# Optimization experiments

Hardware: AMD Instinct MI355X
Metric: run time of the kernel (lower is better)

## Reference

```python
import jax, jax.numpy as jnp
import numpy as np

N = 50000      # num nodes
E = 800000     # num edges (avg degree 16)
IN, H, OUT = 128, 128, 16
R = 8          # num relations


def rgcn_conv(x, edge_index, edge_type, W, root, bias, num_relations):
    """PyG RGCNConv with aggr='mean': out = x@root + bias + sum_r mean_{j in N_r(i)} x_j @ W_r.
    Mean is linear, so aggregate raw x_j per relation first, then one matmul per relation."""
    src, dst = edge_index[0], edge_index[1]  # messages flow src -> dst
    x_src = x[src]                            # [E, F] gather
    out = x @ root + bias                     # root/self term
    for r in range(num_relations):            # small fixed loop over relations
        m = (edge_type == r).astype(x.dtype)  # [E]
        s = jax.ops.segment_sum(x_src * m[:, None], dst, num_segments=x.shape[0])  # [N, F]
        c = jax.ops.segment_sum(m, dst, num_segments=x.shape[0])                   # [N]
        out = out + (s / jnp.maximum(c, 1.0)[:, None]) @ W[r]
    return out


def setup_inputs() -> dict:
    key = jax.random.key(0)
    ks = jax.random.split(key, 12)
    glorot = lambda k, shape: jax.random.normal(k, shape, jnp.float32) * (2.0 / (shape[-2] + shape[-1])) ** 0.5
    return {
        "x": jax.random.normal(ks[0], (N, IN), jnp.float32),
        "edge_index": jax.random.randint(ks[1], (2, E), 0, N, jnp.int64) if jax.config.read('jax_enable_x64') else jax.random.randint(ks[1], (2, E), 0, N).astype(jnp.int32),
        "edge_type": jax.random.randint(ks[2], (E,), 0, R).astype(jnp.int32),
        "w0": glorot(ks[3], (R, IN, H)),
        "root0": glorot(ks[4], (IN, H)),
        "b0": jnp.zeros((H,), jnp.float32),
        "w1": glorot(ks[5], (R, H, H)),
        "root1": glorot(ks[6], (H, H)),
        "b1": jnp.zeros((H,), jnp.float32),
        "w2": glorot(ks[7], (R, H, OUT)),
        "root2": glorot(ks[8], (H, OUT)),
        "b2": jnp.zeros((OUT,), jnp.float32),
    }


def reference(x, edge_index, edge_type, w0, root0, b0, w1, root1, b1, w2, root2, b2):
    # layer 0: in -> hidden, relu (dropout is identity in eval mode)
    h = jax.nn.relu(rgcn_conv(x, edge_index, edge_type, w0, root0, b0, R))
    # layer 1: hidden -> hidden, relu
    h = jax.nn.relu(rgcn_conv(h, edge_index, edge_type, w1, root1, b1, R))
    # layer 2: hidden -> out (no activation)
    return rgcn_conv(h, edge_index, edge_type, w2, root2, b2, R)
```

## Files before the change

kernel.cpp:

```cpp
#include <hip/hip_runtime.h>

#define N_NODES 50000
#define N_EDGES 800000
#define NREL 8
#define NB8 (N_NODES * NREL)
#define SCAN_T 12500
#define KSTEPS 36
#define A_STRIDE 1160
#define NTILES (N_NODES / 16)

typedef __attribute__((ext_vector_type(8))) short short8;
typedef __attribute__((ext_vector_type(4))) float f32x4;
typedef __attribute__((ext_vector_type(2))) float f32x2;

__device__ __forceinline__ unsigned short f2bf(float v) {
    union { float f; unsigned int u; } c; c.f = v;
    return (unsigned short)((c.u + 0x7FFFu + ((c.u >> 16) & 1u)) >> 16);
}
__device__ __forceinline__ float bfhi2f(unsigned int u) {
    union { unsigned int u; float f; } c; c.u = u & 0xFFFF0000u; return c.f;
}
__device__ __forceinline__ float bflo2f(unsigned int u) {
    union { unsigned int u; float f; } c; c.u = u << 16; return c.f;
}

#define PREP_Z   (NB8 / 4)
#define PREP_X   (N_NODES * 32)
#define PREP_P   (8 * KSTEPS * 64)
#define PREP_P2  (1 * KSTEPS * 64)
#define PREP_TOTAL (PREP_Z + PREP_X + 2 * PREP_P + PREP_P2)

__device__ __forceinline__ void pack_one(int idx, const float* __restrict__ root,
                                         const float* __restrict__ W,
                                         unsigned short* __restrict__ Wpack, int FOUT) {
    int lane = idx & 63;
    int ks = (idx >> 6) % KSTEPS;
    int ct = idx / (KSTEPS * 64);
    int kbase = ks * 32 + (lane >> 4) * 8;
    int col = ct * 16 + (lane & 15);
    union { unsigned short us[8]; uint4 v; } u;
#pragma unroll
    for (int j = 0; j < 8; j++) {
        int k = kbase + j;
        float val = (k < 128) ? root[(size_t)k * FOUT + col]
                              : W[(size_t)(k - 128) * FOUT + col];
        u.us[j] = f2bf(val);
    }
    ((uint4*)Wpack)[idx] = u.v;
}

__global__ void prep_kernel(const float* __restrict__ X, unsigned int* __restrict__ Xb2,
                            const float* __restrict__ r0, const float* __restrict__ w0,
                            unsigned short* __restrict__ Wp0,
                            const float* __restrict__ r1, const float* __restrict__ w1,
                            unsigned short* __restrict__ Wp1,
                            const float* __restrict__ r2, const float* __restrict__ w2,
                            unsigned short* __restrict__ Wp2,
                            int* __restrict__ cnt) {
    int t = blockIdx.x * blockDim.x + threadIdx.x;
    if (t < PREP_Z) { ((int4*)cnt)[t] = make_int4(0, 0, 0, 0); return; }
    t -= PREP_Z;
    if (t < PREP_X) {
        float4 v = ((const float4*)X)[t];
        unsigned int p0 = (unsigned int)f2bf(v.x) | ((unsigned int)f2bf(v.y) << 16);
        unsigned int p1 = (unsigned int)f2bf(v.z) | ((unsigned int)f2bf(v.w) << 16);
        ((uint2*)Xb2)[t] = make_uint2(p0, p1);
        return;
    }
    t -= PREP_X;
    if (t < PREP_P) { pack_one(t, r0, w0, Wp0, 128); return; }
    t -= PREP_P;
    if (t < PREP_P) { pack_one(t, r1, w1, Wp1, 128); return; }
    t -= PREP_P;
    if (t < PREP_P2) pack_one(t, r2, w2, Wp2, 16);
}

__global__ void rank_kernel(const int* __restrict__ ei, const int* __restrict__ et,
                            int* __restrict__ cnt, int* __restrict__ rank, int E) {
    int e = blockIdx.x * blockDim.x + threadIdx.x;
    if (e >= E) return;
    int d = ei[E + e];
    int t = et[e];
    rank[e] = atomicAdd(&cnt[d * NREL + t], 1);
}

__global__ void scanA_kernel(const int* __restrict__ cnt, int* __restrict__ tsum) {
    int g = blockIdx.x * blockDim.x + threadIdx.x;
    if (g >= SCAN_T) return;
    const int4* p = (const int4*)(cnt + (size_t)g * 32);
    int s = 0;
#pragma unroll
    for (int j = 0; j < 8; j++) {
        int4 v = p[j];
        s += v.x + v.y + v.z + v.w;
    }
    tsum[g] = s;
}

__global__ void scanB_kernel(const int* __restrict__ tsum, int* __restrict__ toff) {
    __shared__ int part[1024];
    int t = threadIdx.x;
    const int C = 13;
    int n0 = t * C, n1 = n0 + C; if (n1 > SCAN_T) n1 = SCAN_T;
    int s = 0;
    for (int n = n0; n < n1; n++) s += tsum[n];
    part[t] = s;
    __syncthreads();
    for (int off = 1; off < 1024; off <<= 1) {
        int v = (t >= off) ? part[t - off] : 0;
        __syncthreads();
        part[t] += v;
        __syncthreads();
    }
    int run = (t > 0) ? part[t - 1] : 0;
    for (int n = n0; n < n1; n++) { toff[n] = run; run += tsum[n]; }
}

__global__ void scanC_kernel(const int* __restrict__ cnt, const int* __restrict__ toff,
                             int* __restrict__ rs8) {
    int g = blockIdx.x * blockDim.x + threadIdx.x;
    if (g >= SCAN_T) return;
    int run = toff[g];
    int base = g * 32;
#pragma unroll 4
    for (int j = 0; j < 32; j++) {
        rs8[base + j] = run;
        run += cnt[base + j];
    }
    if (g == 0) rs8[NB8] = N_EDGES;
}

__global__ void place_kernel(const int* __restrict__ ei, const int* __restrict__ et,
                             const int* __restrict__ rank, const int* __restrict__ rs8,
                             unsigned short* __restrict__ csr_src, int E) {
    int e = blockIdx.x * blockDim.x + threadIdx.x;
    if (e >= E) return;
    int s = ei[e];
    int d = ei[E + e];
    int t = et[e];
    csr_src[rs8[d * NREL + t] + rank[e]] = (unsigned short)s;
}

template <int FOUT, bool RELU>
__global__ __launch_bounds__(512, 8) void layer_kernel(
    const unsigned int* __restrict__ Xb2,
    const int* __restrict__ rs8,
    const unsigned short* __restrict__ csr_src,
    const unsigned short* __restrict__ Wpack,
    const float* __restrict__ bias,
    void* __restrict__ Yout)
{
    __shared__ __align__(16) unsigned short Abuf[16][A_STRIDE];

    int tid = threadIdx.x;
    int wave = tid >> 6, lane = tid & 63;
    int l15 = lane & 15;
    int node0 = blockIdx.x * 16;

    {
        int gn0 = node0 + wave * 2;
        unsigned int* row0 = (unsigned int*)&Abuf[wave * 2][0];
        unsigned int* row1 = (unsigned int*)&Abuf[wave * 2 + 1][0];

        int bl = lane <= 16 ? lane : 16;
        int bv = rs8[gn0 * 8 + bl];
        unsigned int self0 = Xb2[(size_t)gn0 * 64 + lane];
        unsigned int self1 = Xb2[(size_t)(gn0 + 1) * 64 + lane];

        int e     = __builtin_amdgcn_readlane(bv, 0);
        int e_end = __builtin_amdgcn_readlane(bv, 16);

        row0[lane] = self0;
        row1[lane] = self1;

        int r = 0;
        int segs = e;
        int be = __builtin_amdgcn_readlane(bv, 1);
        f32x2 av = (f32x2){0.f, 0.f};

#define FLUSH_R()                                                              \
        do {                                                                   \
            int c_ = be - segs;                                                \
            float iv_ = 1.0f / (float)(c_ > 0 ? c_ : 1);                       \
            unsigned int pk_ = (unsigned int)f2bf(av.x * iv_)                  \
                             | ((unsigned int)f2bf(av.y * iv_) << 16);         \
            unsigned int* rw_ = (r < 8) ? row0 : row1;                         \
            rw_[(1 + (r & 7)) * 64 + lane] = pk_;                              \
            av = (f32x2){0.f, 0.f}; segs = be; r++;                            \
            be = __builtin_amdgcn_readlane(bv, r + 1 <= 16 ? r + 1 : 16);      \
        } while (0)

        if (e < e_end) {
            int e1m = e_end - 1;
            int ma = e + l15; if (ma > e1m) ma = e1m;
            unsigned int mv = csr_src[ma];
            while (e < e_end) {
                int bn = e_end - e; if (bn > 16) bn = 16;
                int sc[16];
#pragma unroll
                for (int k = 0; k < 16; k++) sc[k] = __builtin_amdgcn_readlane((int)mv, k);
                unsigned int xp[16];
#pragma unroll
                for (int k = 0; k < 16; k++) xp[k] = Xb2[(size_t)sc[k] * 64 + lane];
                int en = e + bn;
                if (en < e_end) {
                    int mb = en + l15; if (mb > e1m) mb = e1m;
                    mv = csr_src[mb];
                }
#pragma unroll
                for (int k = 0; k < 16; k++) {
                    if (k < bn) {
                        int ec = e + k;
                        while (ec >= be) FLUSH_R();
                        av += (f32x2){bflo2f(xp[k]), bfhi2f(xp[k])};
                    }
                }
                e = en;
            }
        }
        while (r < 16) FLUSH_R();
#undef FLUSH_R
    }
    __syncthreads();

    int quad = lane >> 4, l16 = lane & 15;
    if constexpr (FOUT == 128) {
        int ct = wave;
        f32x4 acc = (f32x4){0.f, 0.f, 0.f, 0.f};
        for (int ks = 0; ks < KSTEPS; ks++) {
            short8 b = *(const short8*)(Wpack + (((size_t)ct * KSTEPS + ks) * 64 + lane) * 8);
            short8 a = *(const short8*)&Abuf[l16][ks * 32 + quad * 8];
            acc = __builtin_amdgcn_mfma_f32_16x16x32_bf16(a, b, acc, 0, 0, 0);
        }
        unsigned short* Yb = (unsigned short*)Yout;
        int h = ct * 16 + l16;
        float bvs = bias[h];
#pragma unroll
        for (int r4 = 0; r4 < 4; r4++) {
            int node = node0 + quad * 4 + r4;
            float v = acc[r4] + bvs;
            if (RELU) v = v > 0.f ? v : 0.f;
            Yb[(size_t)node * 128 + h] = f2bf(v);
        }
    } else {
        int ks0 = wave * 4 + (wave < 4 ? wave : 4);
        int ksn = (wave < 4) ? 5 : 4;
        f32x4 acc = (f32x4){0.f, 0.f, 0.f, 0.f};
        for (int ks = ks0; ks < ks0 + ksn; ks++) {
            short8 b = *(const short8*)(Wpack + ((size_t)ks * 64 + lane) * 8);
            short8 a = *(const short8*)&Abuf[l16][ks * 32 + quad * 8];
            acc = __builtin_amdgcn_mfma_f32_16x16x32_bf16(a, b, acc, 0, 0, 0);
        }
        __syncthreads();
        float* red = (float*)&Abuf[0][0];
#pragma unroll
        for (int r4 = 0; r4 < 4; r4++) red[(wave * 64 + lane) * 4 + r4] = acc[r4];
        __syncthreads();
        if (tid < 256) {
            int reg = tid >> 6, l = tid & 63;
            float s = 0.f;
#pragma unroll
            for (int w = 0; w < 8; w++) s += red[(w * 64 + l) * 4 + reg];
            int node = node0 + ((l >> 4) << 2) + reg;
            int h = l & 15;
            float v = s + bias[h];
            if (RELU) v = v > 0.f ? v : 0.f;
            ((float*)Yout)[(size_t)node * 16 + h] = v;
        }
    }
}

extern "C" void kernel_launch(void* const* d_in, const int* in_sizes, int n_in,
                              void* d_out, int out_size, void* d_ws, size_t ws_size,
                              hipStream_t stream) {
    const float* x  = (const float*)d_in[0];
    const int*   ei = (const int*)d_in[1];
    const int*   et = (const int*)d_in[2];
    const float* w0 = (const float*)d_in[3];
    const float* r0 = (const float*)d_in[4];
    const float* b0 = (const float*)d_in[5];
    const float* w1 = (const float*)d_in[6];
    const float* r1 = (const float*)d_in[7];
    const float* b1 = (const float*)d_in[8];
    const float* w2 = (const float*)d_in[9];
    const float* r2 = (const float*)d_in[10];
    const float* b2 = (const float*)d_in[11];

    char* wsp = (char*)d_ws;
    size_t off = 0;
    auto alloc = [&](size_t bytes) -> void* {
        void* p = wsp + off;
        off += (bytes + 255) & ~(size_t)255;
        return p;
    };

    int* cnt    = (int*)alloc((size_t)NB8 * 4);
    int* rs8    = (int*)alloc(((size_t)NB8 + 1) * 4);
    int* rank   = (int*)alloc((size_t)N_EDGES * 4);
    int* tsum   = (int*)alloc((size_t)SCAN_T * 4);
    int* toff   = (int*)alloc((size_t)SCAN_T * 4);
    unsigned short* csr_src = (unsigned short*)alloc((size_t)N_EDGES * 2);
    unsigned short* Wp0 = (unsigned short*)alloc((size_t)8 * KSTEPS * 64 * 8 * 2);
    unsigned short* Wp1 = (unsigned short*)alloc((size_t)8 * KSTEPS * 64 * 8 * 2);
    unsigned short* Wp2 = (unsigned short*)alloc((size_t)1 * KSTEPS * 64 * 8 * 2);
    unsigned int* Xb = (unsigned int*)alloc((size_t)N_NODES * 64 * 4);
    unsigned int* H0 = (unsigned int*)alloc((size_t)N_NODES * 64 * 4);
    unsigned int* H1 = (unsigned int*)alloc((size_t)N_NODES * 64 * 4);

    prep_kernel<<<dim3((PREP_TOTAL + 255) / 256), dim3(256), 0, stream>>>(
        x, Xb, r0, w0, Wp0, r1, w1, Wp1, r2, w2, Wp2, cnt);
    rank_kernel<<<dim3((N_EDGES + 255) / 256), dim3(256), 0, stream>>>(ei, et, cnt, rank, N_EDGES);
    scanA_kernel<<<dim3((SCAN_T + 255) / 256), dim3(256), 0, stream>>>(cnt, tsum);
    scanB_kernel<<<dim3(1), dim3(1024), 0, stream>>>(tsum, toff);
    scanC_kernel<<<dim3((SCAN_T + 255) / 256), dim3(256), 0, stream>>>(cnt, toff, rs8);
    place_kernel<<<dim3((N_EDGES + 255) / 256), dim3(256), 0, stream>>>(ei, et, rank, rs8,
                                                                        csr_src, N_EDGES);

    layer_kernel<128, true ><<<dim3(NTILES), dim3(512), 0, stream>>>(
        Xb, rs8, csr_src, Wp0, b0, (void*)H0);
    layer_kernel<128, true ><<<dim3(NTILES), dim3(512), 0, stream>>>(
        H0, rs8, csr_src, Wp1, b1, (void*)H1);
    layer_kernel<16, false><<<dim3(NTILES), dim3(512), 0, stream>>>(
        H1, rs8, csr_src, Wp2, b2, d_out);
}
```

Baseline: 322.4 us.

## Warp-specialize layer kernel with double-buffered producer/consumer tiles and fuse scan kernels

The layer kernel now processes several 16-node tiles per block. Four producer waves gather and mean-aggregate neighbour features into one of two shared buffers while four consumer waves run the MFMA GEMM on the other buffer. The aim is to overlap gather latency with matrix math and to drop the cross-wave reduction in the FOUT=16 layer. Separately, the three scan kernels become one kernel that uses global atomic flags as a grid barrier, which removes two launches. That barrier relies on all 49 blocks being resident at the same time, and each layer kernel now has only half its waves doing the gather.

```diff
diff --git a/kernel.cpp b/kernel.cpp
--- a/kernel.cpp
+++ b/kernel.cpp
@@ -6,8 +6,10 @@
 #define NB8 (N_NODES * NREL)
 #define SCAN_T 12500
 #define KSTEPS 36
-#define A_STRIDE 1160
+#define AROW_D 580
 #define NTILES (N_NODES / 16)
+#define TPB 6
+#define LGRID ((NTILES + TPB - 1) / TPB)
 
 typedef __attribute__((ext_vector_type(8))) short short8;
 typedef __attribute__((ext_vector_type(4))) float f32x4;
@@ -56,8 +58,9 @@
                             unsigned short* __restrict__ Wp1,
                             const float* __restrict__ r2, const float* __restrict__ w2,
                             unsigned short* __restrict__ Wp2,
-                            int* __restrict__ cnt) {
+                            int* __restrict__ cnt, int* __restrict__ flags) {
     int t = blockIdx.x * blockDim.x + threadIdx.x;
+    if (blockIdx.x == 0 && threadIdx.x < 4) flags[threadIdx.x] = 0;
     if (t < PREP_Z) { ((int4*)cnt)[t] = make_int4(0, 0, 0, 0); return; }
     t -= PREP_Z;
     if (t < PREP_X) {
@@ -84,50 +87,59 @@
     rank[e] = atomicAdd(&cnt[d * NREL + t], 1);
 }
 
-__global__ void scanA_kernel(const int* __restrict__ cnt, int* __restrict__ tsum) {
-    int g = blockIdx.x * blockDim.x + threadIdx.x;
-    if (g >= SCAN_T) return;
-    const int4* p = (const int4*)(cnt + (size_t)g * 32);
-    int s = 0;
-#pragma unroll
-    for (int j = 0; j < 8; j++) {
-        int4 v = p[j];
-        s += v.x + v.y + v.z + v.w;
-    }
-    tsum[g] = s;
-}
-
-__global__ void scanB_kernel(const int* __restrict__ tsum, int* __restrict__ toff) {
-    __shared__ int part[1024];
-    int t = threadIdx.x;
-    const int C = 13;
-    int n0 = t * C, n1 = n0 + C; if (n1 > SCAN_T) n1 = SCAN_T;
-    int s = 0;
-    for (int n = n0; n < n1; n++) s += tsum[n];
-    part[t] = s;
+#define SCAN_BLOCKS 49
+__global__ __launch_bounds__(256) void scanABC_kernel(
+    const int* __restrict__ cnt, int* __restrict__ tsum, int* __restrict__ toff,
+    int* __restrict__ rs8, int* __restrict__ flags) {
+    int tid = threadIdx.x;
+    int gstride = SCAN_BLOCKS * 256;
+    for (int g = blockIdx.x * 256 + tid; g < SCAN_T; g += gstride) {
+        const int4* p = (const int4*)(cnt + (size_t)g * 32);
+        int s = 0;
+#pragma unroll
+        for (int j = 0; j < 8; j++) {
+            int4 v = p[j];
+            s += v.x + v.y + v.z + v.w;
+        }
+        tsum[g] = s;
+    }
+    __threadfence();
     __syncthreads();
-    for (int off = 1; off < 1024; off <<= 1) {
-        int v = (t >= off) ? part[t - off] : 0;
+    if (tid == 0) atomicAdd(&flags[0], 1);
+    if (blockIdx.x == 0) {
+        __shared__ int part[256];
+        if (tid == 0) { while (atomicAdd(&flags[0], 0) < SCAN_BLOCKS) {} __threadfence(); }
         __syncthreads();
-        part[t] += v;
+        const int C = (SCAN_T + 255) / 256;
+        int n0 = tid * C, n1 = n0 + C; if (n1 > SCAN_T) n1 = SCAN_T;
+        int s = 0;
+        for (int n = n0; n < n1; n++) s += tsum[n];
+        part[tid] = s;
         __syncthreads();
-    }
-    int run = (t > 0) ? part[t - 1] : 0;
-    for (int n = n0; n < n1; n++) { toff[n] = run; run += tsum[n]; }
-}
-
-__global__ void scanC_kernel(const int* __restrict__ cnt, const int* __restrict__ toff,
-                             int* __restrict__ rs8) {
-    int g = blockIdx.x * blockDim.x + threadIdx.x;
-    if (g >= SCAN_T) return;
-    int run = toff[g];
-    int base = g * 32;
+        for (int off = 1; off < 256; off <<= 1) {
+            int v = (tid >= off) ? part[tid - off] : 0;
+            __syncthreads();
+            part[tid] += v;
+            __syncthreads();
+        }
+        int run = (tid > 0) ? part[tid - 1] : 0;
+        for (int n = n0; n < n1; n++) { toff[n] = run; run += tsum[n]; }
+        __threadfence();
+        __syncthreads();
+        if (tid == 0) atomicAdd(&flags[1], 1);
+    }
+    if (tid == 0) { while (atomicAdd(&flags[1], 0) < 1) {} __threadfence(); }
+    __syncthreads();
+    for (int g = blockIdx.x * 256 + tid; g < SCAN_T; g += gstride) {
+        int run = toff[g];
+        int base = g * 32;
 #pragma unroll 4
-    for (int j = 0; j < 32; j++) {
-        rs8[base + j] = run;
-        run += cnt[base + j];
-    }
-    if (g == 0) rs8[NB8] = N_EDGES;
+        for (int j = 0; j < 32; j++) {
+            rs8[base + j] = run;
+            run += cnt[base + j];
+        }
+    }
+    if (blockIdx.x == 0 && tid == 0) rs8[NB8] = N_EDGES;
 }
 
 __global__ void place_kernel(const int* __restrict__ ei, const int* __restrict__ et,
@@ -142,7 +154,7 @@
 }
 
 template <int FOUT, bool RELU>
-__global__ __launch_bounds__(512, 8) void layer_kernel(
+__global__ __launch_bounds__(512, 4) void layer_kernel(
     const unsigned int* __restrict__ Xb2,
     const int* __restrict__ rs8,
     const unsigned short* __restrict__ csr_src,
@@ -150,28 +162,28 @@
     const float* __restrict__ bias,
     void* __restrict__ Yout)
 {
-    __shared__ __align__(16) unsigned short Abuf[16][A_STRIDE];
+    __shared__ __align__(16) unsigned int Abuf[2][16][AROW_D];
 
     int tid = threadIdx.x;
     int wave = tid >> 6, lane = tid & 63;
     int l15 = lane & 15;
-    int node0 = blockIdx.x * 16;
-
-    {
-        int gn0 = node0 + wave * 2;
-        unsigned int* row0 = (unsigned int*)&Abuf[wave * 2][0];
-        unsigned int* row1 = (unsigned int*)&Abuf[wave * 2 + 1][0];
-
-        int bl = lane <= 16 ? lane : 16;
+    int quad = lane >> 4, l16 = lane & 15;
+    bool producer = wave < 4;
+
+    auto produce = [&](int buf, int tile) {
+        int gn0 = tile * 16 + wave * 4;
+        int bl = lane <= 32 ? lane : 32;
         int bv = rs8[gn0 * 8 + bl];
-        unsigned int self0 = Xb2[(size_t)gn0 * 64 + lane];
-        unsigned int self1 = Xb2[(size_t)(gn0 + 1) * 64 + lane];
-
+        unsigned int s0 = Xb2[((unsigned)(gn0 + 0) << 6) | lane];
+        unsigned int s1 = Xb2[((unsigned)(gn0 + 1) << 6) | lane];
+        unsigned int s2 = Xb2[((unsigned)(gn0 + 2) << 6) | lane];
+        unsigned int s3 = Xb2[((unsigned)(gn0 + 3) << 6) | lane];
         int e     = __builtin_amdgcn_readlane(bv, 0);
-        int e_end = __builtin_amdgcn_readlane(bv, 16);
-
-        row0[lane] = self0;
-        row1[lane] = self1;
+        int e_end = __builtin_amdgcn_readlane(bv, 32);
+        Abuf[buf][wave * 4 + 0][lane] = s0;
+        Abuf[buf][wave * 4 + 1][lane] = s1;
+        Abuf[buf][wave * 4 + 2][lane] = s2;
+        Abuf[buf][wave * 4 + 3][lane] = s3;
 
         int r = 0;
         int segs = e;
@@ -184,10 +196,9 @@
             float iv_ = 1.0f / (float)(c_ > 0 ? c_ : 1);                       \
             unsigned int pk_ = (unsigned int)f2bf(av.x * iv_)                  \
                              | ((unsigned int)f2bf(av.y * iv_) << 16);         \
-            unsigned int* rw_ = (r < 8) ? row0 : row1;                         \
-            rw_[(1 + (r & 7)) * 64 + lane] = pk_;                              \
+            Abuf[buf][wave * 4 + (r >> 3)][(1 + (r & 7)) * 64 + lane] = pk_;   \
             av = (f32x2){0.f, 0.f}; segs = be; r++;                            \
-            be = __builtin_amdgcn_readlane(bv, r + 1 <= 16 ? r + 1 : 16);      \
+            be = __builtin_amdgcn_readlane(bv, r + 1 <= 32 ? r + 1 : 32);      \
         } while (0)
 
         if (e < e_end) {
@@ -201,7 +212,8 @@
                 for (int k = 0; k < 16; k++) sc[k] = __builtin_amdgcn_readlane((int)mv, k);
                 unsigned int xp[16];
 #pragma unroll
-                for (int k = 0; k < 16; k++) xp[k] = Xb2[(size_t)sc[k] * 64 + lane];
+                for (int k = 0; k < 16; k++)
+                    xp[k] = Xb2[((unsigned)sc[k] << 6) | lane];
                 int en = e + bn;
                 if (en < e_end) {
                     int mb = en + l15; if (mb > e1m) mb = e1m;
@@ -218,55 +230,73 @@
                 e = en;
             }
         }
-        while (r < 16) FLUSH_R();
+        while (r < 32) FLUSH_R();
 #undef FLUSH_R
-    }
+    };
+
+    auto consume = [&](int buf, int tile) {
+        int node0 = tile * 16;
+        const unsigned short* arow = (const unsigned short*)&Abuf[buf][l16][0];
+        if constexpr (FOUT == 128) {
+            int c = wave - 4;
+            int ct0 = c, ct1 = c + 4;
+            f32x4 acc0 = (f32x4){0.f, 0.f, 0.f, 0.f};
+            f32x4 acc1 = (f32x4){0.f, 0.f, 0.f, 0.f};
+            const uint4* bp0 = (const uint4*)Wpack + (size_t)ct0 * KSTEPS * 64 + lane;
+            const uint4* bp1 = (const uint4*)Wpack + (size_t)ct1 * KSTEPS * 64 + lane;
+            for (int ks = 0; ks < KSTEPS; ks++) {
+                short8 a = *(const short8*)(arow + ks * 32 + quad * 8);
+                short8 b0 = *(const short8*)(bp0 + ks * 64);
+                short8 b1 = *(const short8*)(bp1 + ks * 64);
+                acc0 = __builtin_amdgcn_mfma_f32_16x16x32_bf16(a, b0, acc0, 0, 0, 0);
+                acc1 = __builtin_amdgcn_mfma_f32_16x16x32_bf16(a, b1, acc1, 0, 0, 0);
+            }
+            unsigned short* Yb = (unsigned short*)Yout;
+            int h0 = ct0 * 16 + l16, h1 = ct1 * 16 + l16;
+            float bv0 = bias[h0], bv1 = bias[h1];
+#pragma unroll
+            for (int r4 = 0; r4 < 4; r4++) {
+                int node = node0 + quad * 4 + r4;
+                float v0 = acc0[r4] + bv0;
+                float v1 = acc1[r4] + bv1;
+                if (RELU) { v0 = v0 > 0.f ? v0 : 0.f; v1 = v1 > 0.f ? v1 : 0.f; }
+                Yb[(size_t)node * 128 + h0] = f2bf(v0);
+                Yb[(size_t)node * 128 + h1] = f2bf(v1);
+            }
+        } else {
+            if (wave == 4) {
+                f32x4 acc = (f32x4){0.f, 0.f, 0.f, 0.f};
+                const uint4* bp = (const uint4*)Wpack + lane;
+                for (int ks = 0; ks < KSTEPS; ks++) {
+                    short8 a = *(const short8*)(arow + ks * 32 + quad * 8);
+                    short8 b = *(const short8*)(bp + ks * 64);
+                    acc = __builtin_amdgcn_mfma_f32_16x16x32_bf16(a, b, acc, 0, 0, 0);
+                }
+                int h = l16;
+                float bvs = bias[h];
+#pragma unroll
+                for (int r4 = 0; r4 < 4; r4++) {
+                    int node = node0 + quad * 4 + r4;
+                    float v = acc[r4] + bvs;
+                    if (RELU) v = v > 0.f ? v : 0.f;
+                    ((float*)Yout)[(size_t)node * 16 + h] = v;
+                }
+            }
+        }
+    };
+
+    int tbase = blockIdx.x * TPB;
+    if (producer && tbase < NTILES) produce(0, tbase);
     __syncthreads();
-
-    int quad = lane >> 4, l16 = lane & 15;
-    if constexpr (FOUT == 128) {
-        int ct = wave;
-        f32x4 acc = (f32x4){0.f, 0.f, 0.f, 0.f};
-        for (int ks = 0; ks < KSTEPS; ks++) {
-            short8 b = *(const short8*)(Wpack + (((size_t)ct * KSTEPS + ks) * 64 + lane) * 8);
-            short8 a = *(const short8*)&Abuf[l16][ks * 32 + quad * 8];
-            acc = __builtin_amdgcn_mfma_f32_16x16x32_bf16(a, b, acc, 0, 0, 0);
-        }
-        unsigned short* Yb = (unsigned short*)Yout;
-        int h = ct * 16 + l16;
-        float bvs = bias[h];
-#pragma unroll
-        for (int r4 = 0; r4 < 4; r4++) {
-            int node = node0 + quad * 4 + r4;
-            float v = acc[r4] + bvs;
-            if (RELU) v = v > 0.f ? v : 0.f;
-            Yb[(size_t)node * 128 + h] = f2bf(v);
-        }
-    } else {
-        int ks0 = wave * 4 + (wave < 4 ? wave : 4);
-        int ksn = (wave < 4) ? 5 : 4;
-        f32x4 acc = (f32x4){0.f, 0.f, 0.f, 0.f};
-        for (int ks = ks0; ks < ks0 + ksn; ks++) {
-            short8 b = *(const short8*)(Wpack + ((size_t)ks * 64 + lane) * 8);
-            short8 a = *(const short8*)&Abuf[l16][ks * 32 + quad * 8];
-            acc = __builtin_amdgcn_mfma_f32_16x16x32_bf16(a, b, acc, 0, 0, 0);
+    for (int s = 0; s < TPB; s++) {
+        int tcur = tbase + s;
+        if (producer) {
+            int tnext = tcur + 1;
+            if (s + 1 < TPB && tnext < NTILES) produce((s + 1) & 1, tnext);
+        } else {
+            if (tcur < NTILES) consume(s & 1, tcur);
         }
         __syncthreads();
-        float* red = (float*)&Abuf[0][0];
-#pragma unroll
-        for (int r4 = 0; r4 < 4; r4++) red[(wave * 64 + lane) * 4 + r4] = acc[r4];
-        __syncthreads();
-        if (tid < 256) {
-            int reg = tid >> 6, l = tid & 63;
-            float s = 0.f;
-#pragma unroll
-            for (int w = 0; w < 8; w++) s += red[(w * 64 + l) * 4 + reg];
-            int node = node0 + ((l >> 4) << 2) + reg;
-            int h = l & 15;
-            float v = s + bias[h];
-            if (RELU) v = v > 0.f ? v : 0.f;
-            ((float*)Yout)[(size_t)node * 16 + h] = v;
-        }
     }
 }
 
@@ -299,6 +329,7 @@
     int* rank   = (int*)alloc((size_t)N_EDGES * 4);
     int* tsum   = (int*)alloc((size_t)SCAN_T * 4);
     int* toff   = (int*)alloc((size_t)SCAN_T * 4);
+    int* flags  = (int*)alloc(4 * 4);
     unsigned short* csr_src = (unsigned short*)alloc((size_t)N_EDGES * 2);
     unsigned short* Wp0 = (unsigned short*)alloc((size_t)8 * KSTEPS * 64 * 8 * 2);
     unsigned short* Wp1 = (unsigned short*)alloc((size_t)8 * KSTEPS * 64 * 8 * 2);
@@ -308,18 +339,16 @@
     unsigned int* H1 = (unsigned int*)alloc((size_t)N_NODES * 64 * 4);
 
     prep_kernel<<<dim3((PREP_TOTAL + 255) / 256), dim3(256), 0, stream>>>(
-        x, Xb, r0, w0, Wp0, r1, w1, Wp1, r2, w2, Wp2, cnt);
+        x, Xb, r0, w0, Wp0, r1, w1, Wp1, r2, w2, Wp2, cnt, flags);
     rank_kernel<<<dim3((N_EDGES + 255) / 256), dim3(256), 0, stream>>>(ei, et, cnt, rank, N_EDGES);
-    scanA_kernel<<<dim3((SCAN_T + 255) / 256), dim3(256), 0, stream>>>(cnt, tsum);
-    scanB_kernel<<<dim3(1), dim3(1024), 0, stream>>>(tsum, toff);
-    scanC_kernel<<<dim3((SCAN_T + 255) / 256), dim3(256), 0, stream>>>(cnt, toff, rs8);
+    scanABC_kernel<<<dim3(SCAN_BLOCKS), dim3(256), 0, stream>>>(cnt, tsum, toff, rs8, flags);
     place_kernel<<<dim3((N_EDGES + 255) / 256), dim3(256), 0, stream>>>(ei, et, rank, rs8,
                                                                         csr_src, N_EDGES);
 
-    layer_kernel<128, true ><<<dim3(NTILES), dim3(512), 0, stream>>>(
+    layer_kernel<128, true ><<<dim3(LGRID), dim3(512), 0, stream>>>(
         Xb, rs8, csr_src, Wp0, b0, (void*)H0);
-    layer_kernel<128, true ><<<dim3(NTILES), dim3(512), 0, stream>>>(
+    layer_kernel<128, true ><<<dim3(LGRID), dim3(512), 0, stream>>>(
         H0, rs8, csr_src, Wp1, b1, (void*)H1);
-    layer_kernel<16, false><<<dim3(NTILES), dim3(512), 0, stream>>>(
+    layer_kernel<16, false><<<dim3(LGRID), dim3(512), 0, stream>>>(
         H1, rs8, csr_src, Wp2, b2, d_out);
 }
```

New measurement: 670.7 us. 108% more time.
